# Performance work log

Measured on AMD Instinct MI355X. Metric: run time of the kernel, lower is better.

## Reference

```python
import jax, jax.numpy as jnp
import numpy as np

HID = 256   # hiddenDims
QD = 64     # queryDims
B = 16      # number of segments
LQ = 2048   # query tokens per segment
LH = 2048   # key/value tokens per segment
EPS = 1e-5


def _layer_norm(x, w, b):
    m = jnp.mean(x, axis=-1, keepdims=True)
    v = jnp.mean((x - m) ** 2, axis=-1, keepdims=True)
    return (x - m) / jnp.sqrt(v + EPS) * w + b


def setup_inputs() -> dict:
    key = jax.random.key(0)
    ks = jax.random.split(key, 8)
    q = jax.random.normal(ks[0], (B * LQ, HID), jnp.float32)
    h = jax.random.normal(ks[1], (B * LH, HID), jnp.float32)
    s = 1.0 / np.sqrt(HID)
    WQ = jax.random.normal(ks[2], (QD, HID), jnp.float32) * s
    WK = jax.random.normal(ks[3], (QD, HID), jnp.float32) * s
    WV = jax.random.normal(ks[4], (HID, HID), jnp.float32) * s
    fc_w = jax.random.normal(ks[5], (HID, HID), jnp.float32) * s
    fc_b = jax.random.normal(ks[6], (HID,), jnp.float32) * 0.01
    norm0_w = jnp.ones((HID,), jnp.float32)
    norm0_b = jnp.zeros((HID,), jnp.float32)
    norm1_w = jnp.ones((HID,), jnp.float32)
    norm1_b = jnp.zeros((HID,), jnp.float32)
    qlens = jnp.full((B,), LQ, jnp.int32)
    hlens = jnp.full((B,), LH, jnp.int32)
    return {"q": q, "h": h, "WQ": WQ, "WK": WK, "WV": WV,
            "fc_w": fc_w, "fc_b": fc_b,
            "norm0_w": norm0_w, "norm0_b": norm0_b,
            "norm1_w": norm1_w, "norm1_b": norm1_b,
            "qlens": qlens, "hlens": hlens}


def reference(q, h, WQ, WK, WV, fc_w, fc_b,
              norm0_w, norm0_b, norm1_w, norm1_b, qlens, hlens):
    # segments are equal-length, so the ragged per-segment loop is exactly
    # batched block-diagonal attention over [B, L, D] views.
    nb = qlens.shape[0]
    Lq = q.shape[0] // nb
    Lh = h.shape[0] // hlens.shape[0]
    D = q.shape[-1]
    qq = (q @ WQ.T).reshape(nb, Lq, -1)          # [B, Lq, QD]
    k = (h @ WK.T).reshape(nb, Lh, -1)           # [B, Lh, QD]
    v = (h @ WV.T).reshape(nb, Lh, D)            # [B, Lh, D]
    scale = 1.0 / jnp.sqrt(jnp.asarray(qq.shape[-1], jnp.float32))
    a = jax.nn.softmax(jnp.einsum('bqc,bkc->bqk', qq, k) * scale, axis=-1)
    att = jnp.einsum('bqk,bkd->bqd', a, v).reshape(-1, D)  # concat of segments
    x = _layer_norm(q + att, norm0_w, norm0_b)
    hres = x @ fc_w.T + fc_b
    return _layer_norm(x + jax.nn.relu(hres), norm1_w, norm1_b)
```

## Files before the change

### kernel.cpp

```cpp
#include <hip/hip_runtime.h>
#include <hip/hip_bf16.h>

#define HID 256
#define QD 64
#define NSEG 16
#define SLQ 2048
#define SLH 2048


typedef __attribute__((ext_vector_type(8))) short bf16x8;
typedef __attribute__((ext_vector_type(8))) __bf16 bf16x8b;
typedef __attribute__((ext_vector_type(4))) float f32x4;
typedef __attribute__((ext_vector_type(4))) short s16x4;

#define BAR_LDS() asm volatile("s_waitcnt lgkmcnt(0)\n\ts_barrier" ::: "memory")

static __device__ __forceinline__ f32x4 mfma16(bf16x8 a, bf16x8 b, f32x4 c) {
  return __builtin_amdgcn_mfma_f32_16x16x32_bf16(
      __builtin_bit_cast(bf16x8b, a), __builtin_bit_cast(bf16x8b, b), c, 0, 0, 0);
}

static __device__ __forceinline__ short f2bf(float x) {
  union { float f; unsigned u; } v; v.f = x;
  unsigned r = v.u + 0x7fffu + ((v.u >> 16) & 1u);
  return (short)(r >> 16);
}

static __device__ __forceinline__ float bf2f(short s) {
  union { unsigned u; float f; } v;
  v.u = ((unsigned)(unsigned short)s) << 16;
  return v.f;
}

static __device__ __forceinline__ void pack_w(const float* __restrict__ s,
                                              short* __restrict__ d, int i) {
  int j = i & 7, l16 = (i >> 3) & 15, quad = (i >> 7) & 3, ks = (i >> 9) & 7,
      n = i >> 12;
  d[i] = f2bf(s[(size_t)(n * 16 + l16) * HID + ks * 32 + quad * 8 + j]);
}

__global__ __launch_bounds__(256) void cast4_kernel(const float* __restrict__ s0, short* __restrict__ d0, int n0,
                                                    const float* __restrict__ s1, short* __restrict__ d1, int n1,
                                                    const float* __restrict__ s2, short* __restrict__ d2, int n2,
                                                    const float* __restrict__ s3, short* __restrict__ d3, int n3) {
  int i = blockIdx.x * 256 + threadIdx.x;
  if (i < n0) pack_w(s0, d0, i);
  int j = i - n0;
  if (j >= 0 && j < n1) pack_w(s1, d1, j);
  int k = j - n1;
  if (k >= 0 && k < n2) pack_w(s2, d2, k);
  int l = k - n2;
  if (l >= 0 && l < n3) pack_w(s3, d3, l);
}

__global__ __launch_bounds__(256, 4) void proj_kv_kernel(const float* __restrict__ h,
                                                         const short* __restrict__ wkb,
                                                         const short* __restrict__ wvb,
                                                         short* __restrict__ kb,
                                                         short* __restrict__ vt) {
  __shared__ short hb[64][264];
  int wave = threadIdx.x >> 6, lane = threadIdx.x & 63;
  int quad = lane >> 4, l16 = lane & 15;
  int mw = wave * 16;
  int m0 = blockIdx.x * 64;
#pragma unroll
  for (int i = 0; i < 16; ++i) {
    int idx = i * 256 + threadIdx.x;
    int row = idx >> 6, col = (idx & 63) * 4;
    f32x4 v = *(const f32x4*)(h + (size_t)(m0 + row) * HID + col);
    s16x4 pk;
#pragma unroll
    for (int j = 0; j < 4; ++j) pk[j] = f2bf(v[j]);
    *(s16x4*)&hb[row][col] = pk;
  }
  __syncthreads();
  f32x4 kacc[4];
  f32x4 vacc[16];
#pragma unroll
  for (int n = 0; n < 4; ++n) kacc[n] = f32x4{0.f, 0.f, 0.f, 0.f};
#pragma unroll
  for (int n = 0; n < 16; ++n) vacc[n] = f32x4{0.f, 0.f, 0.f, 0.f};
#pragma unroll
  for (int ks = 0; ks < 8; ++ks) {
    bf16x8 a = *(const bf16x8*)&hb[mw + l16][ks * 32 + quad * 8];
#pragma unroll
    for (int n = 0; n < 4; ++n) {
      bf16x8 b = *(const bf16x8*)(wkb + (size_t)((n * 8 + ks) * 64 + lane) * 8);
      kacc[n] = mfma16(a, b, kacc[n]);
    }
#pragma unroll
    for (int mt = 0; mt < 16; ++mt) {
      bf16x8 wf = *(const bf16x8*)(wvb + (size_t)((mt * 8 + ks) * 64 + lane) * 8);
      vacc[mt] = mfma16(wf, a, vacc[mt]);
    }
  }
  {
    char* kx = (char*)&hb[mw][0];
#pragma unroll
    for (int n = 0; n < 4; ++n)
#pragma unroll
      for (int r = 0; r < 4; ++r) {
        int k16 = quad * 4 + r;
        int bo = (k16 * 128 + (n * 16 + l16) * 2) ^ ((k16 & 7) << 4);
        *(short*)(kx + bo) = f2bf(kacc[n][r]);
      }
    asm volatile("s_waitcnt lgkmcnt(0)" ::: "memory");
    int seg = (m0 + mw) >> 11;
    int g = ((m0 + mw) & 2047) >> 4;
    short* kdst = kb + (size_t)seg * 131072 + (size_t)g * 1024 + lane * 8;
#pragma unroll
    for (int p = 0; p < 2; ++p) {
      int bo = (l16 * 128 + p * 64 + quad * 16) ^ ((l16 & 7) << 4);
      *(bf16x8*)(kdst + p * 512) = *(bf16x8*)(kx + bo);
    }
  }
  __syncthreads();
  {
    char* vbuf = (char*)&hb[0][0];
#pragma unroll
    for (int mt = 0; mt < 16; ++mt)
#pragma unroll
      for (int r = 0; r < 4; ++r) {
        int dv = mt * 16 + quad * 4 + r;
        int bo = (dv * 128 + (mw + l16) * 2) ^ ((dv & 7) << 4);
        *(short*)(vbuf + bo) = f2bf(vacc[mt][r]);
      }
    __syncthreads();
    int seg = m0 >> 11;
    int t0 = m0 & 2047;
    int kt = t0 >> 7;
    int ksb = (t0 >> 5) & 3;
    short* vdst = vt + (size_t)seg * 524288;
#pragma unroll
    for (int i = 0; i < 8; ++i) {
      int u = wave * 8 + i;
      int ksl = u >> 4, d16 = u & 15;
      int dim = d16 * 16 + l16;
      int bo = (dim * 128 + ksl * 64 + quad * 16) ^ ((dim & 7) << 4);
      size_t unit = (size_t)((kt * 4 + ksb + ksl) * 16 + d16);
      *(bf16x8*)(vdst + unit * 512 + lane * 8) = *(bf16x8*)(vbuf + bo);
    }
  }
}

__global__ __launch_bounds__(512, 4) void attn_kernel(const float* __restrict__ q,
                                                      const short* __restrict__ wqb,
                                                      const short* __restrict__ kb,
                                                      const short* __restrict__ vt,
                                                      const short* __restrict__ fwb,
                                                      const float* __restrict__ fcb,
                                                      const float* __restrict__ n0w,
                                                      const float* __restrict__ n0b,
                                                      const float* __restrict__ n1w,
                                                      const float* __restrict__ n1b,
                                                      float* __restrict__ out) {
  __shared__ short p_lds[2][64][136];
  __shared__ short qx[4096];
  __shared__ float plsum[4][2][16];
  __shared__ float rs[2][2][64];
  int wave = threadIdx.x >> 6, lane = threadIdx.x & 63;
  int quad = lane >> 4, l16 = lane & 15;
  int qg = wave >> 1, kh = wave & 1;
  int b = blockIdx.x;
  int xcd = b & 7, li = b >> 3;
  int seg = xcd * 2 + (li >> 5);
  int tile = li & 31;
  int qrow0 = seg * SLQ + tile * 64;
  const short* kseg = kb + (size_t)seg * 131072;
  const short* vseg = vt + (size_t)seg * 524288;

  const float cexp = 0.125f * 1.44269504f;
  bf16x8 kpre[4][2];

#define LOADK(KT)                                                               \
  {                                                                             \
    _Pragma("unroll") for (int t = 0; t < 4; ++t) {                             \
      const short* kp = kseg + (size_t)((KT) * 8 + kh * 4 + t) * 1024 + lane * 8;\
      kpre[t][0] = *(const bf16x8*)kp;                                          \
      kpre[t][1] = *(const bf16x8*)(kp + 512);                                  \
    }                                                                           \
  }

  LOADK(tile & 15)

  short (*st)[264] = (short(*)[264]) & p_lds[0][0][0];
  bf16x8 qf0, qf1;
  {
    const float* qsrc = q + (size_t)qrow0 * HID;
#pragma unroll
    for (int i = 0; i < 8; ++i) {
      int idx = i * 512 + threadIdx.x;
      int row = idx >> 6, col = (idx & 63) * 4;
      f32x4 v = *(const f32x4*)(qsrc + (size_t)row * HID + col);
      s16x4 pk;
#pragma unroll
      for (int j = 0; j < 4; ++j) pk[j] = f2bf(v[j]);
      *(s16x4*)&st[row][col] = pk;
    }
    __syncthreads();
    f32x4 qacc[2];
    qacc[0] = f32x4{0.f, 0.f, 0.f, 0.f};
    qacc[1] = f32x4{0.f, 0.f, 0.f, 0.f};
#pragma unroll
    for (int ks = 0; ks < 8; ++ks) {
      bf16x8 a = *(const bf16x8*)&st[qg * 16 + l16][ks * 32 + quad * 8];
#pragma unroll
      for (int ni = 0; ni < 2; ++ni) {
        int n = kh * 2 + ni;
        bf16x8 wb = *(const bf16x8*)(wqb + (size_t)((n * 8 + ks) * 64 + lane) * 8);
        qacc[ni] = mfma16(a, wb, qacc[ni]);
      }
    }
    BAR_LDS();
#pragma unroll
    for (int ni = 0; ni < 2; ++ni)
#pragma unroll
      for (int r = 0; r < 4; ++r) {
        int n = kh * 2 + ni;
        int colp = (n & 1) * 16 + l16;
        qx[(qg * 2 + (n >> 1)) * 512 + ((colp >> 3) * 16 + quad * 4 + r) * 8 +
           (colp & 7)] = f2bf(qacc[ni][r]);
      }
    BAR_LDS();
    const short* qxp = qx + qg * 1024 + lane * 8;
    qf0 = *(const bf16x8*)qxp;
    qf1 = *(const bf16x8*)(qxp + 512);
  }

  f32x4 o[4][2];
#pragma unroll
  for (int m = 0; m < 4; ++m)
#pragma unroll
    for (int n = 0; n < 2; ++n) o[m][n] = f32x4{0.f, 0.f, 0.f, 0.f};
  float lsum = 0.f;

#define S_PHASE(BUF)                                                            \
  {                                                                             \
    f32x4 s[4];                                                                 \
    _Pragma("unroll") for (int t = 0; t < 4; ++t) {                             \
      f32x4 a = f32x4{0.f, 0.f, 0.f, 0.f};                                      \
      a = mfma16(kpre[t][0], qf0, a);                                           \
      a = mfma16(kpre[t][1], qf1, a);                                           \
      s[t] = a;                                                                 \
    }                                                                           \
    _Pragma("unroll") for (int t = 0; t < 4; ++t) {                             \
      float p0 = __builtin_amdgcn_exp2f(s[t][0] * cexp);                        \
      float p1 = __builtin_amdgcn_exp2f(s[t][1] * cexp);                        \
      float p2 = __builtin_amdgcn_exp2f(s[t][2] * cexp);                        \
      float p3 = __builtin_amdgcn_exp2f(s[t][3] * cexp);                        \
      lsum += (p0 + p1) + (p2 + p3);                                            \
      s16x4 pk;                                                                 \
      pk[0] = f2bf(p0); pk[1] = f2bf(p1); pk[2] = f2bf(p2); pk[3] = f2bf(p3);   \
      *(s16x4*)&p_lds[BUF][qg * 16 + l16][kh * 64 + t * 16 + quad * 4] = pk;    \
    }                                                                           \
  }

#define PV_PHASE(KT, BUF)                                                       \
  {                                                                             \
    _Pragma("unroll") for (int ks = 0; ks < 4; ++ks) {                          \
      bf16x8 pf[4];                                                             \
      _Pragma("unroll") for (int m = 0; m < 4; ++m)                             \
        pf[m] = *(const bf16x8*)&p_lds[BUF][m * 16 + l16][ks * 32 + quad * 8];  \
      _Pragma("unroll") for (int n = 0; n < 2; ++n) {                           \
        const short* vp = vseg +                                                \
            ((size_t)((KT) * 4 + ks) * 16 + wave * 2 + n) * 512 + lane * 8;     \
        bf16x8 vf = *(const bf16x8*)vp;                                         \
        _Pragma("unroll") for (int m = 0; m < 4; ++m)                           \
          o[m][n] = mfma16(pf[m], vf, o[m][n]);                                 \
      }                                                                         \
    }                                                                           \
  }

  S_PHASE(0)
  LOADK((tile + 1) & 15)
  BAR_LDS();
#pragma unroll 1
  for (int j = 1; j < 16; ++j) {
    S_PHASE(j & 1)
    if (j < 15) LOADK((tile + j + 1) & 15)
    PV_PHASE((tile + j - 1) & 15, (j - 1) & 1)
    BAR_LDS();
  }
  PV_PHASE((tile + 15) & 15, 1)

  lsum += __shfl_xor(lsum, 16);
  lsum += __shfl_xor(lsum, 32);

  BAR_LDS();
  if (lane < 16) plsum[qg][kh][lane] = lsum;
  short (*ob)[264] = (short(*)[264]) & p_lds[0][0][0];
#pragma unroll
  for (int m = 0; m < 4; ++m)
#pragma unroll
    for (int n = 0; n < 2; ++n)
#pragma unroll
      for (int r = 0; r < 4; ++r)
        ob[m * 16 + quad * 4 + r][wave * 32 + n * 16 + l16] = f2bf(o[m][n][r]);
  BAR_LDS();

  {
    int row = wave * 8 + (lane >> 3);
    int c0 = (lane & 7) * 32;
    float linv = 1.f / (plsum[row >> 4][0][row & 15] + plsum[row >> 4][1][row & 15]);
    float y[32];
    float s1 = 0.f, s2 = 0.f;
    const float* qp = q + (size_t)(qrow0 + row) * HID + c0;
#pragma unroll
    for (int k = 0; k < 4; ++k) {
      bf16x8 ov = *(const bf16x8*)&ob[row][c0 + k * 8];
      f32x4 qa = *(const f32x4*)(qp + k * 8);
      f32x4 qb = *(const f32x4*)(qp + k * 8 + 4);
#pragma unroll
      for (int j = 0; j < 4; ++j) {
        float yv = qa[j] + bf2f(ov[j]) * linv;
        y[k * 8 + j] = yv;
        s1 += yv; s2 += yv * yv;
      }
#pragma unroll
      for (int j = 0; j < 4; ++j) {
        float yv = qb[j] + bf2f(ov[4 + j]) * linv;
        y[k * 8 + 4 + j] = yv;
        s1 += yv; s2 += yv * yv;
      }
    }
    s1 += __shfl_xor(s1, 1); s2 += __shfl_xor(s2, 1);
    s1 += __shfl_xor(s1, 2); s2 += __shfl_xor(s2, 2);
    s1 += __shfl_xor(s1, 4); s2 += __shfl_xor(s2, 4);
    float mean = s1 * (1.f / HID);
    float var = s2 * (1.f / HID) - mean * mean;
    float rstd = rsqrtf(var + 1e-5f);
#pragma unroll
    for (int k = 0; k < 4; ++k) {
      f32x4 wa = *(const f32x4*)(n0w + c0 + k * 8);
      f32x4 wb = *(const f32x4*)(n0w + c0 + k * 8 + 4);
      f32x4 ba = *(const f32x4*)(n0b + c0 + k * 8);
      f32x4 bb = *(const f32x4*)(n0b + c0 + k * 8 + 4);
      s16x4 o0, o1;
#pragma unroll
      for (int j = 0; j < 4; ++j) {
        o0[j] = f2bf((y[k * 8 + j] - mean) * rstd * wa[j] + ba[j]);
        o1[j] = f2bf((y[k * 8 + 4 + j] - mean) * rstd * wb[j] + bb[j]);
      }
      *(s16x4*)&ob[row][c0 + k * 8] = o0;
      *(s16x4*)&ob[row][c0 + k * 8 + 4] = o1;
    }
  }
  BAR_LDS();

  {
    f32x4 facc[8];
#pragma unroll
    for (int n2 = 0; n2 < 8; ++n2) facc[n2] = f32x4{0.f, 0.f, 0.f, 0.f};
#pragma unroll
    for (int ks = 0; ks < 8; ++ks) {
      bf16x8 a = *(const bf16x8*)&ob[qg * 16 + l16][ks * 32 + quad * 8];
#pragma unroll
      for (int n2 = 0; n2 < 8; ++n2) {
        int n = kh * 8 + n2;
        bf16x8 wb = *(const bf16x8*)(fwb + (size_t)((n * 8 + ks) * 64 + lane) * 8);
        facc[n2] = mfma16(a, wb, facc[n2]);
      }
    }
#pragma unroll
    for (int r = 0; r < 4; ++r) {
      int row = qg * 16 + quad * 4 + r;
      float s = 0.f, s2 = 0.f;
#pragma unroll
      for (int n2 = 0; n2 < 8; ++n2) {
        int col = kh * 128 + n2 * 16 + l16;
        float hres = fmaxf(facc[n2][r] + fcb[col], 0.f);
        float yv = bf2f(ob[row][col]) + hres;
        s += yv; s2 += yv * yv;
      }
      s += __shfl_xor(s, 1); s2 += __shfl_xor(s2, 1);
      s += __shfl_xor(s, 2); s2 += __shfl_xor(s2, 2);
      s += __shfl_xor(s, 4); s2 += __shfl_xor(s2, 4);
      s += __shfl_xor(s, 8); s2 += __shfl_xor(s2, 8);
      if (l16 == 0) { rs[0][kh][row] = s; rs[1][kh][row] = s2; }
    }
    BAR_LDS();
#pragma unroll
    for (int r = 0; r < 4; ++r) {
      int row = qg * 16 + quad * 4 + r;
      float st1 = rs[0][0][row] + rs[0][1][row];
      float st2 = rs[1][0][row] + rs[1][1][row];
      float mean = st1 * (1.f / HID);
      float var = st2 * (1.f / HID) - mean * mean;
      float rstd = rsqrtf(var + 1e-5f);
      float* op = out + (size_t)(qrow0 + row) * HID;
#pragma unroll
      for (int n2 = 0; n2 < 8; ++n2) {
        int col = kh * 128 + n2 * 16 + l16;
        float hres = fmaxf(facc[n2][r] + fcb[col], 0.f);
        float yv = bf2f(ob[row][col]) + hres;
        op[col] = (yv - mean) * rstd * n1w[col] + n1b[col];
      }
    }
  }
#undef LOADK
#undef S_PHASE
#undef PV_PHASE
}

extern "C" void kernel_launch(void* const* d_in, const int* in_sizes, int n_in,
                              void* d_out, int out_size, void* d_ws, size_t ws_size,
                              hipStream_t stream) {
  const float* q = (const float*)d_in[0];
  const float* h = (const float*)d_in[1];
  const float* WQ = (const float*)d_in[2];
  const float* WK = (const float*)d_in[3];
  const float* WV = (const float*)d_in[4];
  const float* fc_w = (const float*)d_in[5];
  const float* fc_b = (const float*)d_in[6];
  const float* n0w = (const float*)d_in[7];
  const float* n0b = (const float*)d_in[8];
  const float* n1w = (const float*)d_in[9];
  const float* n1b = (const float*)d_in[10];

  char* ws = (char*)d_ws;
  short* kb = (short*)(ws);
  short* vt = (short*)(ws + ((size_t)4 << 20));
  short* wqb = (short*)(ws + ((size_t)20 << 20));
  short* wkb = (short*)(ws + ((size_t)20 << 20) + 32 * 1024);
  short* wvb = (short*)(ws + ((size_t)20 << 20) + 64 * 1024);
  short* fwb = (short*)(ws + ((size_t)20 << 20) + 192 * 1024);

  cast4_kernel<<<640, 256, 0, stream>>>(WQ, wqb, QD * HID, WK, wkb, QD * HID,
                                        WV, wvb, HID * HID, fc_w, fwb, HID * HID);
  proj_kv_kernel<<<512, 256, 0, stream>>>(h, wkb, wvb, kb, vt);
  attn_kernel<<<512, 512, 0, stream>>>(q, wqb, kb, vt, fwb, fc_b,
                                       n0w, n0b, n1w, n1b, (float*)d_out);
}
```

Measured before the change: 245.2 us.

## Fuse weight cast, KV projection and attention into one kernel with grid barriers

Merges the three launches (weight packing, K/V projection, attention plus epilogue) into a single persistent kernel of 512 blocks that separates the phases with software grid barriers built on atomics. The KV projection is re-split across 8 waves, with four waves doing K and all eight sharing V. The goal is to remove launch gaps and inter-kernel drain/fill cost. In exchange it adds a memset and two global spin barriers, and it relies on all 512 blocks being co-resident, which would deadlock if occupancy were insufficient.

New measurement: 286.1 us. +16.7%, slower.

```diff
diff --git a/kernel.cpp b/kernel.cpp
--- a/kernel.cpp
+++ b/kernel.cpp
@@ -39,129 +39,142 @@
   d[i] = f2bf(s[(size_t)(n * 16 + l16) * HID + ks * 32 + quad * 8 + j]);
 }
 
-__global__ __launch_bounds__(256) void cast4_kernel(const float* __restrict__ s0, short* __restrict__ d0, int n0,
-                                                    const float* __restrict__ s1, short* __restrict__ d1, int n1,
-                                                    const float* __restrict__ s2, short* __restrict__ d2, int n2,
-                                                    const float* __restrict__ s3, short* __restrict__ d3, int n3) {
-  int i = blockIdx.x * 256 + threadIdx.x;
-  if (i < n0) pack_w(s0, d0, i);
-  int j = i - n0;
-  if (j >= 0 && j < n1) pack_w(s1, d1, j);
-  int k = j - n1;
-  if (k >= 0 && k < n2) pack_w(s2, d2, k);
-  int l = k - n2;
-  if (l >= 0 && l < n3) pack_w(s3, d3, l);
-}
-
-__global__ __launch_bounds__(256, 4) void proj_kv_kernel(const float* __restrict__ h,
-                                                         const short* __restrict__ wkb,
-                                                         const short* __restrict__ wvb,
-                                                         short* __restrict__ kb,
-                                                         short* __restrict__ vt) {
-  __shared__ short hb[64][264];
-  int wave = threadIdx.x >> 6, lane = threadIdx.x & 63;
-  int quad = lane >> 4, l16 = lane & 15;
-  int mw = wave * 16;
-  int m0 = blockIdx.x * 64;
-#pragma unroll
-  for (int i = 0; i < 16; ++i) {
-    int idx = i * 256 + threadIdx.x;
-    int row = idx >> 6, col = (idx & 63) * 4;
-    f32x4 v = *(const f32x4*)(h + (size_t)(m0 + row) * HID + col);
-    s16x4 pk;
-#pragma unroll
-    for (int j = 0; j < 4; ++j) pk[j] = f2bf(v[j]);
-    *(s16x4*)&hb[row][col] = pk;
-  }
+static __device__ __forceinline__ void grid_barrier(unsigned* cnt,
+                                                    unsigned* flag,
+                                                    unsigned nblk) {
   __syncthreads();
-  f32x4 kacc[4];
-  f32x4 vacc[16];
-#pragma unroll
-  for (int n = 0; n < 4; ++n) kacc[n] = f32x4{0.f, 0.f, 0.f, 0.f};
-#pragma unroll
-  for (int n = 0; n < 16; ++n) vacc[n] = f32x4{0.f, 0.f, 0.f, 0.f};
-#pragma unroll
-  for (int ks = 0; ks < 8; ++ks) {
-    bf16x8 a = *(const bf16x8*)&hb[mw + l16][ks * 32 + quad * 8];
-#pragma unroll
-    for (int n = 0; n < 4; ++n) {
-      bf16x8 b = *(const bf16x8*)(wkb + (size_t)((n * 8 + ks) * 64 + lane) * 8);
-      kacc[n] = mfma16(a, b, kacc[n]);
-    }
-#pragma unroll
-    for (int mt = 0; mt < 16; ++mt) {
-      bf16x8 wf = *(const bf16x8*)(wvb + (size_t)((mt * 8 + ks) * 64 + lane) * 8);
-      vacc[mt] = mfma16(wf, a, vacc[mt]);
-    }
-  }
-  {
-    char* kx = (char*)&hb[mw][0];
-#pragma unroll
-    for (int n = 0; n < 4; ++n)
-#pragma unroll
-      for (int r = 0; r < 4; ++r) {
-        int k16 = quad * 4 + r;
-        int bo = (k16 * 128 + (n * 16 + l16) * 2) ^ ((k16 & 7) << 4);
-        *(short*)(kx + bo) = f2bf(kacc[n][r]);
-      }
-    asm volatile("s_waitcnt lgkmcnt(0)" ::: "memory");
-    int seg = (m0 + mw) >> 11;
-    int g = ((m0 + mw) & 2047) >> 4;
-    short* kdst = kb + (size_t)seg * 131072 + (size_t)g * 1024 + lane * 8;
-#pragma unroll
-    for (int p = 0; p < 2; ++p) {
-      int bo = (l16 * 128 + p * 64 + quad * 16) ^ ((l16 & 7) << 4);
-      *(bf16x8*)(kdst + p * 512) = *(bf16x8*)(kx + bo);
-    }
+  if (threadIdx.x == 0) {
+    __threadfence();
+    unsigned old = atomicAdd(cnt, 1u);
+    if (old == nblk - 1u) {
+      atomicExch(flag, 1u);
+    } else {
+      while (atomicAdd(flag, 0u) == 0u) __builtin_amdgcn_s_sleep(2);
+    }
+    __threadfence();
   }
   __syncthreads();
-  {
-    char* vbuf = (char*)&hb[0][0];
-#pragma unroll
-    for (int mt = 0; mt < 16; ++mt)
-#pragma unroll
-      for (int r = 0; r < 4; ++r) {
-        int dv = mt * 16 + quad * 4 + r;
-        int bo = (dv * 128 + (mw + l16) * 2) ^ ((dv & 7) << 4);
-        *(short*)(vbuf + bo) = f2bf(vacc[mt][r]);
-      }
-    __syncthreads();
-    int seg = m0 >> 11;
-    int t0 = m0 & 2047;
-    int kt = t0 >> 7;
-    int ksb = (t0 >> 5) & 3;
-    short* vdst = vt + (size_t)seg * 524288;
-#pragma unroll
-    for (int i = 0; i < 8; ++i) {
-      int u = wave * 8 + i;
-      int ksl = u >> 4, d16 = u & 15;
-      int dim = d16 * 16 + l16;
-      int bo = (dim * 128 + ksl * 64 + quad * 16) ^ ((dim & 7) << 4);
-      size_t unit = (size_t)((kt * 4 + ksb + ksl) * 16 + d16);
-      *(bf16x8*)(vdst + unit * 512 + lane * 8) = *(bf16x8*)(vbuf + bo);
-    }
-  }
-}
-
-__global__ __launch_bounds__(512, 4) void attn_kernel(const float* __restrict__ q,
-                                                      const short* __restrict__ wqb,
-                                                      const short* __restrict__ kb,
-                                                      const short* __restrict__ vt,
-                                                      const short* __restrict__ fwb,
-                                                      const float* __restrict__ fcb,
-                                                      const float* __restrict__ n0w,
-                                                      const float* __restrict__ n0b,
-                                                      const float* __restrict__ n1w,
-                                                      const float* __restrict__ n1b,
-                                                      float* __restrict__ out) {
+}
+
+__global__ __launch_bounds__(512, 4) void fused_kernel(
+    const float* __restrict__ q, const float* __restrict__ h,
+    const float* __restrict__ WQ, const float* __restrict__ WK,
+    const float* __restrict__ WV, const float* __restrict__ fcw,
+    const float* __restrict__ fcb, const float* __restrict__ n0w,
+    const float* __restrict__ n0b, const float* __restrict__ n1w,
+    const float* __restrict__ n1b, short* __restrict__ wqb,
+    short* __restrict__ wkb, short* __restrict__ wvb,
+    short* __restrict__ fwb, short* __restrict__ kb,
+    short* __restrict__ vt, unsigned* __restrict__ bar,
+    float* __restrict__ out) {
   __shared__ short p_lds[2][64][136];
   __shared__ short qx[4096];
   __shared__ float plsum[4][2][16];
   __shared__ float rs[2][2][64];
+
   int wave = threadIdx.x >> 6, lane = threadIdx.x & 63;
   int quad = lane >> 4, l16 = lane & 15;
+  int b = blockIdx.x;
+
+  {
+    int gi = b * 512 + threadIdx.x;
+    if (gi < 16384) pack_w(WQ, wqb, gi);
+    else if (gi < 32768) pack_w(WK, wkb, gi - 16384);
+    else if (gi < 98304) pack_w(WV, wvb, gi - 32768);
+    else if (gi < 163840) pack_w(fcw, fwb, gi - 98304);
+  }
+  grid_barrier(bar + 0, bar + 16, 512u);
+
+  {
+    short (*hb)[264] = (short(*)[264]) & p_lds[0][0][0];
+    int m0 = b * 64;
+#pragma unroll
+    for (int i = 0; i < 8; ++i) {
+      int idx = i * 512 + threadIdx.x;
+      int row = idx >> 6, col = (idx & 63) * 4;
+      f32x4 v = *(const f32x4*)(h + (size_t)(m0 + row) * HID + col);
+      s16x4 pk;
+#pragma unroll
+      for (int j = 0; j < 4; ++j) pk[j] = f2bf(v[j]);
+      *(s16x4*)&hb[row][col] = pk;
+    }
+    __syncthreads();
+    int mw = (wave & 3) * 16;
+    int mtb = (wave >> 2) * 8;
+    f32x4 kacc[4];
+    f32x4 vacc[8];
+#pragma unroll
+    for (int n = 0; n < 4; ++n) kacc[n] = f32x4{0.f, 0.f, 0.f, 0.f};
+#pragma unroll
+    for (int n = 0; n < 8; ++n) vacc[n] = f32x4{0.f, 0.f, 0.f, 0.f};
+#pragma unroll
+    for (int ks = 0; ks < 8; ++ks) {
+      bf16x8 a = *(const bf16x8*)&hb[mw + l16][ks * 32 + quad * 8];
+      if (wave < 4) {
+#pragma unroll
+        for (int n = 0; n < 4; ++n) {
+          bf16x8 wb = *(const bf16x8*)(wkb + (size_t)((n * 8 + ks) * 64 + lane) * 8);
+          kacc[n] = mfma16(a, wb, kacc[n]);
+        }
+      }
+#pragma unroll
+      for (int mt = 0; mt < 8; ++mt) {
+        bf16x8 wf = *(const bf16x8*)(wvb + (size_t)(((mtb + mt) * 8 + ks) * 64 + lane) * 8);
+        vacc[mt] = mfma16(wf, a, vacc[mt]);
+      }
+    }
+    __syncthreads();
+    if (wave < 4) {
+      char* kx = (char*)&hb[mw][0];
+#pragma unroll
+      for (int n = 0; n < 4; ++n)
+#pragma unroll
+        for (int r = 0; r < 4; ++r) {
+          int k16 = quad * 4 + r;
+          int bo = (k16 * 128 + (n * 16 + l16) * 2) ^ ((k16 & 7) << 4);
+          *(short*)(kx + bo) = f2bf(kacc[n][r]);
+        }
+      asm volatile("s_waitcnt lgkmcnt(0)" ::: "memory");
+      int seg = (m0 + mw) >> 11;
+      int g = ((m0 + mw) & 2047) >> 4;
+      short* kdst = kb + (size_t)seg * 131072 + (size_t)g * 1024 + lane * 8;
+#pragma unroll
+      for (int p = 0; p < 2; ++p) {
+        int bo = (l16 * 128 + p * 64 + quad * 16) ^ ((l16 & 7) << 4);
+        *(bf16x8*)(kdst + p * 512) = *(bf16x8*)(kx + bo);
+      }
+    }
+    __syncthreads();
+    {
+      char* vbuf = (char*)&hb[0][0];
+#pragma unroll
+      for (int mt = 0; mt < 8; ++mt)
+#pragma unroll
+        for (int r = 0; r < 4; ++r) {
+          int dv = (mtb + mt) * 16 + quad * 4 + r;
+          int bo = (dv * 128 + (mw + l16) * 2) ^ ((dv & 7) << 4);
+          *(short*)(vbuf + bo) = f2bf(vacc[mt][r]);
+        }
+      __syncthreads();
+      int seg = m0 >> 11;
+      int t0 = m0 & 2047;
+      int kt = t0 >> 7;
+      int ksb = (t0 >> 5) & 3;
+      short* vdst = vt + (size_t)seg * 524288;
+#pragma unroll
+      for (int i = 0; i < 4; ++i) {
+        int u = wave * 4 + i;
+        int ksl = u >> 4, d16 = u & 15;
+        int dim = d16 * 16 + l16;
+        int bo = (dim * 128 + ksl * 64 + quad * 16) ^ ((dim & 7) << 4);
+        size_t unit = (size_t)((kt * 4 + ksb + ksl) * 16 + d16);
+        *(bf16x8*)(vdst + unit * 512 + lane * 8) = *(bf16x8*)(vbuf + bo);
+      }
+    }
+  }
+  grid_barrier(bar + 32, bar + 48, 512u);
+
   int qg = wave >> 1, kh = wave & 1;
-  int b = blockIdx.x;
   int xcd = b & 7, li = b >> 3;
   int seg = xcd * 2 + (li >> 5);
   int tile = li & 31;
@@ -424,10 +437,10 @@
   short* wkb = (short*)(ws + ((size_t)20 << 20) + 32 * 1024);
   short* wvb = (short*)(ws + ((size_t)20 << 20) + 64 * 1024);
   short* fwb = (short*)(ws + ((size_t)20 << 20) + 192 * 1024);
-
-  cast4_kernel<<<640, 256, 0, stream>>>(WQ, wqb, QD * HID, WK, wkb, QD * HID,
-                                        WV, wvb, HID * HID, fc_w, fwb, HID * HID);
-  proj_kv_kernel<<<512, 256, 0, stream>>>(h, wkb, wvb, kb, vt);
-  attn_kernel<<<512, 512, 0, stream>>>(q, wqb, kb, vt, fwb, fc_b,
-                                       n0w, n0b, n1w, n1b, (float*)d_out);
-}
+  unsigned* bar = (unsigned*)(ws + ((size_t)21 << 20));
+
+  hipMemsetAsync(bar, 0, 256, stream);
+  fused_kernel<<<512, 512, 0, stream>>>(q, h, WQ, WK, WV, fc_w, fc_b,
+                                        n0w, n0b, n1w, n1b, wqb, wkb, wvb,
+                                        fwb, kb, vt, bar, (float*)d_out);
+}
```

## Stage V tiles into LDS with async global_load_lds and halve key tile

Applied to the files above, without the earlier changes.

The attention loop now walks keys in 64-key steps (32 iterations) instead of 128-key steps. V fragments are no longer read from global memory inside the PV phase. Each wave prefetches them one step ahead into an LDS slab with async direct-to-LDS loads, then waits on vmcnt before consuming them. The aim is to hide V global-load latency behind the S-phase work. In exchange, LDS use grows to about 76KB per block, which likely cuts resident blocks per CU, and the loop runs twice as many barriers.

Result: faster. 240.1 us (-2.1%).

```diff
diff --git a/kernel.cpp b/kernel.cpp
--- a/kernel.cpp
+++ b/kernel.cpp
@@ -154,10 +154,13 @@
                                                       const float* __restrict__ n1w,
                                                       const float* __restrict__ n1b,
                                                       float* __restrict__ out) {
-  __shared__ short p_lds[2][64][136];
+  __shared__ __align__(16) char arena_c[67584];
   __shared__ short qx[4096];
   __shared__ float plsum[4][2][16];
   __shared__ float rs[2][2][64];
+  short (*p_lds)[64][72] = (short(*)[64][72])arena_c;
+  short* v_lds = (short*)(arena_c + 34816);
+
   int wave = threadIdx.x >> 6, lane = threadIdx.x & 63;
   int quad = lane >> 4, l16 = lane & 15;
   int qg = wave >> 1, kh = wave & 1;
@@ -170,80 +173,45 @@
   const short* vseg = vt + (size_t)seg * 524288;
 
   const float cexp = 0.125f * 1.44269504f;
-  bf16x8 kpre[4][2];
-
-#define LOADK(KT)                                                               \
+  bf16x8 kpre[2][2];
+
+#define KT2_(J) ((tile * 2 + (J)) & 31)
+
+#define LOADK(KT2)                                                              \
   {                                                                             \
-    _Pragma("unroll") for (int t = 0; t < 4; ++t) {                             \
-      const short* kp = kseg + (size_t)((KT) * 8 + kh * 4 + t) * 1024 + lane * 8;\
+    _Pragma("unroll") for (int t = 0; t < 2; ++t) {                             \
+      const short* kp =                                                         \
+          kseg + (size_t)((KT2) * 4 + kh * 2 + t) * 1024 + lane * 8;            \
       kpre[t][0] = *(const bf16x8*)kp;                                          \
       kpre[t][1] = *(const bf16x8*)(kp + 512);                                  \
     }                                                                           \
   }
 
-  LOADK(tile & 15)
-
-  short (*st)[264] = (short(*)[264]) & p_lds[0][0][0];
-  bf16x8 qf0, qf1;
-  {
-    const float* qsrc = q + (size_t)qrow0 * HID;
-#pragma unroll
-    for (int i = 0; i < 8; ++i) {
-      int idx = i * 512 + threadIdx.x;
-      int row = idx >> 6, col = (idx & 63) * 4;
-      f32x4 v = *(const f32x4*)(qsrc + (size_t)row * HID + col);
-      s16x4 pk;
-#pragma unroll
-      for (int j = 0; j < 4; ++j) pk[j] = f2bf(v[j]);
-      *(s16x4*)&st[row][col] = pk;
-    }
-    __syncthreads();
-    f32x4 qacc[2];
-    qacc[0] = f32x4{0.f, 0.f, 0.f, 0.f};
-    qacc[1] = f32x4{0.f, 0.f, 0.f, 0.f};
-#pragma unroll
-    for (int ks = 0; ks < 8; ++ks) {
-      bf16x8 a = *(const bf16x8*)&st[qg * 16 + l16][ks * 32 + quad * 8];
-#pragma unroll
-      for (int ni = 0; ni < 2; ++ni) {
-        int n = kh * 2 + ni;
-        bf16x8 wb = *(const bf16x8*)(wqb + (size_t)((n * 8 + ks) * 64 + lane) * 8);
-        qacc[ni] = mfma16(a, wb, qacc[ni]);
-      }
-    }
-    BAR_LDS();
-#pragma unroll
-    for (int ni = 0; ni < 2; ++ni)
-#pragma unroll
-      for (int r = 0; r < 4; ++r) {
-        int n = kh * 2 + ni;
-        int colp = (n & 1) * 16 + l16;
-        qx[(qg * 2 + (n >> 1)) * 512 + ((colp >> 3) * 16 + quad * 4 + r) * 8 +
-           (colp & 7)] = f2bf(qacc[ni][r]);
-      }
-    BAR_LDS();
-    const short* qxp = qx + qg * 1024 + lane * 8;
-    qf0 = *(const bf16x8*)qxp;
-    qf1 = *(const bf16x8*)(qxp + 512);
-  }
-
-  f32x4 o[4][2];
-#pragma unroll
-  for (int m = 0; m < 4; ++m)
-#pragma unroll
-    for (int n = 0; n < 2; ++n) o[m][n] = f32x4{0.f, 0.f, 0.f, 0.f};
-  float lsum = 0.f;
+#define VGLL(KT2)                                                               \
+  {                                                                             \
+    _Pragma("unroll") for (int ks = 0; ks < 2; ++ks)                            \
+      _Pragma("unroll") for (int n = 0; n < 2; ++n) {                           \
+        const short* vp = vseg +                                                \
+            ((size_t)((KT2) * 2 + ks) * 16 + wave * 2 + n) * 512 + lane * 8;    \
+        short* lp = v_lds + (((ks * 16 + wave * 2 + n) << 9));                  \
+        __builtin_amdgcn_global_load_lds(                                       \
+            (const __attribute__((address_space(1))) unsigned int*)vp,          \
+            (__attribute__((address_space(3))) unsigned int*)lp, 16, 0, 0);     \
+      }                                                                         \
+  }
+
+#define GUARD_V() asm volatile("s_waitcnt vmcnt(4)" ::: "memory")
 
 #define S_PHASE(BUF)                                                            \
   {                                                                             \
-    f32x4 s[4];                                                                 \
-    _Pragma("unroll") for (int t = 0; t < 4; ++t) {                             \
+    f32x4 s[2];                                                                 \
+    _Pragma("unroll") for (int t = 0; t < 2; ++t) {                             \
       f32x4 a = f32x4{0.f, 0.f, 0.f, 0.f};                                      \
       a = mfma16(kpre[t][0], qf0, a);                                           \
       a = mfma16(kpre[t][1], qf1, a);                                           \
       s[t] = a;                                                                 \
     }                                                                           \
-    _Pragma("unroll") for (int t = 0; t < 4; ++t) {                             \
+    _Pragma("unroll") for (int t = 0; t < 2; ++t) {                             \
       float p0 = __builtin_amdgcn_exp2f(s[t][0] * cexp);                        \
       float p1 = __builtin_amdgcn_exp2f(s[t][1] * cexp);                        \
       float p2 = __builtin_amdgcn_exp2f(s[t][2] * cexp);                        \
@@ -251,44 +219,101 @@
       lsum += (p0 + p1) + (p2 + p3);                                            \
       s16x4 pk;                                                                 \
       pk[0] = f2bf(p0); pk[1] = f2bf(p1); pk[2] = f2bf(p2); pk[3] = f2bf(p3);   \
-      *(s16x4*)&p_lds[BUF][qg * 16 + l16][kh * 64 + t * 16 + quad * 4] = pk;    \
+      *(s16x4*)&p_lds[BUF][qg * 16 + l16][kh * 32 + t * 16 + quad * 4] = pk;    \
     }                                                                           \
   }
 
-#define PV_PHASE(KT, BUF)                                                       \
+#define PV_PHASE(BUF)                                                           \
   {                                                                             \
-    _Pragma("unroll") for (int ks = 0; ks < 4; ++ks) {                          \
+    _Pragma("unroll") for (int ks = 0; ks < 2; ++ks) {                          \
       bf16x8 pf[4];                                                             \
       _Pragma("unroll") for (int m = 0; m < 4; ++m)                             \
         pf[m] = *(const bf16x8*)&p_lds[BUF][m * 16 + l16][ks * 32 + quad * 8];  \
       _Pragma("unroll") for (int n = 0; n < 2; ++n) {                           \
-        const short* vp = vseg +                                                \
-            ((size_t)((KT) * 4 + ks) * 16 + wave * 2 + n) * 512 + lane * 8;     \
-        bf16x8 vf = *(const bf16x8*)vp;                                         \
+        bf16x8 vf = *(const bf16x8*)(v_lds +                                    \
+            ((ks * 16 + wave * 2 + n) << 9) + lane * 8);                        \
         _Pragma("unroll") for (int m = 0; m < 4; ++m)                           \
           o[m][n] = mfma16(pf[m], vf, o[m][n]);                                 \
       }                                                                         \
     }                                                                           \
   }
 
+  LOADK(KT2_(0))
+  VGLL(KT2_(0))
+
+  short (*st)[264] = (short(*)[264])arena_c;
+  bf16x8 qf0, qf1;
+  {
+    const float* qsrc = q + (size_t)qrow0 * HID;
+#pragma unroll
+    for (int i = 0; i < 8; ++i) {
+      int idx = i * 512 + threadIdx.x;
+      int row = idx >> 6, col = (idx & 63) * 4;
+      f32x4 v = *(const f32x4*)(qsrc + (size_t)row * HID + col);
+      s16x4 pk;
+#pragma unroll
+      for (int j = 0; j < 4; ++j) pk[j] = f2bf(v[j]);
+      *(s16x4*)&st[row][col] = pk;
+    }
+    __syncthreads();
+    f32x4 qacc[2];
+    qacc[0] = f32x4{0.f, 0.f, 0.f, 0.f};
+    qacc[1] = f32x4{0.f, 0.f, 0.f, 0.f};
+#pragma unroll
+    for (int ks = 0; ks < 8; ++ks) {
+      bf16x8 a = *(const bf16x8*)&st[qg * 16 + l16][ks * 32 + quad * 8];
+#pragma unroll
+      for (int ni = 0; ni < 2; ++ni) {
+        int n = kh * 2 + ni;
+        bf16x8 wb = *(const bf16x8*)(wqb + (size_t)((n * 8 + ks) * 64 + lane) * 8);
+        qacc[ni] = mfma16(a, wb, qacc[ni]);
+      }
+    }
+    BAR_LDS();
+#pragma unroll
+    for (int ni = 0; ni < 2; ++ni)
+#pragma unroll
+      for (int r = 0; r < 4; ++r) {
+        int n = kh * 2 + ni;
+        int colp = (n & 1) * 16 + l16;
+        qx[(qg * 2 + (n >> 1)) * 512 + ((colp >> 3) * 16 + quad * 4 + r) * 8 +
+           (colp & 7)] = f2bf(qacc[ni][r]);
+      }
+    BAR_LDS();
+    const short* qxp = qx + qg * 1024 + lane * 8;
+    qf0 = *(const bf16x8*)qxp;
+    qf1 = *(const bf16x8*)(qxp + 512);
+  }
+
+  f32x4 o[4][2];
+#pragma unroll
+  for (int m = 0; m < 4; ++m)
+#pragma unroll
+    for (int n = 0; n < 2; ++n) o[m][n] = f32x4{0.f, 0.f, 0.f, 0.f};
+  float lsum = 0.f;
+
   S_PHASE(0)
-  LOADK((tile + 1) & 15)
+  LOADK(KT2_(1))
   BAR_LDS();
 #pragma unroll 1
-  for (int j = 1; j < 16; ++j) {
+  for (int j = 1; j < 32; ++j) {
     S_PHASE(j & 1)
-    if (j < 15) LOADK((tile + j + 1) & 15)
-    PV_PHASE((tile + j - 1) & 15, (j - 1) & 1)
+    if (j < 31) LOADK(KT2_(j + 1))
+    GUARD_V();
+    PV_PHASE((j - 1) & 1)
+    __builtin_amdgcn_sched_barrier(0);
+    VGLL(KT2_(j))
     BAR_LDS();
   }
-  PV_PHASE((tile + 15) & 15, 1)
+  asm volatile("s_waitcnt vmcnt(0)" ::: "memory");
+  PV_PHASE(1)
 
   lsum += __shfl_xor(lsum, 16);
   lsum += __shfl_xor(lsum, 32);
 
   BAR_LDS();
   if (lane < 16) plsum[qg][kh][lane] = lsum;
-  short (*ob)[264] = (short(*)[264]) & p_lds[0][0][0];
+  short (*ob)[264] = (short(*)[264])arena_c;
 #pragma unroll
   for (int m = 0; m < 4; ++m)
 #pragma unroll
@@ -398,8 +423,11 @@
     }
   }
 #undef LOADK
+#undef VGLL
+#undef GUARD_V
 #undef S_PHASE
 #undef PV_PHASE
+#undef KT2_
 }
 
 extern "C" void kernel_launch(void* const* d_in, const int* in_sizes, int n_in,
```
